# Kernel tuning notes

Measured on AMD Instinct MI355X. Metric: run time of the kernel, lower is better.

The kernel has to match this reference:

```python
import jax, jax.numpy as jnp
import numpy as np

N = 8192
IN_F = 512
OUT_F = 64
NEG_SLOPE = 0.01  # nn.LeakyReLU default
MASK_VAL = -1e9


def setup_inputs() -> dict:
    key = jax.random.key(0)
    k_h, k_adj, k_W, k_a = jax.random.split(key, 4)
    h = jax.random.normal(k_h, (N, IN_F), dtype=jnp.float32)
    adjacency = jax.random.randint(k_adj, (N, N), 0, 2, dtype=jnp.int32)
    # xavier_uniform bounds
    bW = float(np.sqrt(6.0 / (IN_F + OUT_F)))
    ba = float(np.sqrt(6.0 / (2 * OUT_F + 1)))
    W = jax.random.uniform(k_W, (IN_F, OUT_F), minval=-bW, maxval=bW, dtype=jnp.float32)
    a = jax.random.uniform(k_a, (2 * OUT_F, 1), minval=-ba, maxval=ba, dtype=jnp.float32)
    return {"h": h, "adjacency": adjacency, "W": W, "a": a}


def reference(h, adjacency, W, a):
    WH = h @ W                                  # [N, out_f]
    wh1 = WH @ a[:OUT_F, :]                     # [N, 1]
    wh2 = WH @ a[OUT_F:, :]                     # [N, 1]
    e = jax.nn.leaky_relu(wh1 + wh2.T, negative_slope=NEG_SLOPE)  # [N, N]
    attnt = jnp.where(adjacency > 0, e, jnp.float32(MASK_VAL))
    attnt = jax.nn.softmax(attnt, axis=1)       # row-wise softmax
    hfirst = attnt @ WH                         # [N, out_f]
    return jax.nn.elu(hfirst)
```

## Files before the change

kernel.cpp:

```cpp
#include <hip/hip_runtime.h>
#include <hip/hip_bf16.h>

#define N 8192
#define IN_F 512
#define OUT_F 64
#define S_SPLIT 16
#define JT (N / S_SPLIT)
#define MP 20

typedef __attribute__((ext_vector_type(8))) short short8;
typedef __attribute__((ext_vector_type(4))) float floatx4;
typedef __attribute__((ext_vector_type(4))) int intx4;

__device__ inline short f2bf(float x) {
    __hip_bfloat16 b = __float2bfloat16(x);
    return __builtin_bit_cast(short, b);
}

__global__ void k_wt(const float* __restrict__ W, short* __restrict__ WT) {
    int idx = blockIdx.x * 256 + threadIdx.x;
    int k = idx >> 6, f = idx & 63;
    WT[f * IN_F + k] = f2bf(W[k * OUT_F + f]);
}

__global__ __launch_bounds__(64) void k_wh(const float* __restrict__ h,
                                           const short* __restrict__ WT,
                                           const float* __restrict__ a,
                                           short* __restrict__ WHbT,
                                           float* __restrict__ wh1,
                                           float* __restrict__ wh2) {
    __shared__ float tile[OUT_F][17];
    int lane = threadIdx.x;
    int n = lane & 15, q = lane >> 4;
    int i0 = blockIdx.x * 16;
    int rowA = i0 + n;
    const float* hp = h + (size_t)rowA * IN_F + q * 8;
    floatx4 acc[4] = {};
    for (int k0 = 0; k0 < IN_F; k0 += 32) {
        floatx4 h0 = *(const floatx4*)(hp + k0);
        floatx4 h1 = *(const floatx4*)(hp + k0 + 4);
        short8 af;
#pragma unroll
        for (int j = 0; j < 4; j++) { af[j] = f2bf(h0[j]); af[j + 4] = f2bf(h1[j]); }
#pragma unroll
        for (int b = 0; b < 4; b++) {
            short8 bf_ = *(const short8*)(WT + (b * 16 + n) * IN_F + k0 + q * 8);
            acc[b] = __builtin_amdgcn_mfma_f32_16x16x32_bf16(af, bf_, acc[b], 0, 0, 0);
        }
    }
#pragma unroll
    for (int b = 0; b < 4; b++)
#pragma unroll
        for (int r = 0; r < 4; r++)
            tile[b * 16 + n][q * 4 + r] = acc[b][r];
    float a1v[4], a2v[4];
#pragma unroll
    for (int b = 0; b < 4; b++) { a1v[b] = a[b * 16 + n]; a2v[b] = a[OUT_F + b * 16 + n]; }
#pragma unroll
    for (int r = 0; r < 4; r++) {
        float s1 = 0.f, s2 = 0.f;
#pragma unroll
        for (int b = 0; b < 4; b++) { s1 += acc[b][r] * a1v[b]; s2 += acc[b][r] * a2v[b]; }
#pragma unroll
        for (int m = 1; m <= 8; m <<= 1) {
            s1 += __shfl_xor(s1, m, 64);
            s2 += __shfl_xor(s2, m, 64);
        }
        if (n == 0) {
            wh1[i0 + q * 4 + r] = s1;
            wh2[i0 + q * 4 + r] = s2;
        }
    }
    __syncthreads();
    const float* tc = tile[lane];
    short8 s0, s1v;
#pragma unroll
    for (int k = 0; k < 8; k++) { s0[k] = f2bf(tc[k]); s1v[k] = f2bf(tc[k + 8]); }
    *(short8*)(WHbT + (size_t)lane * N + i0) = s0;
    *(short8*)(WHbT + (size_t)lane * N + i0 + 8) = s1v;
}

__global__ __launch_bounds__(256) void k_attn(const int* __restrict__ adj,
                                              const short* __restrict__ WHbT,
                                              const float* __restrict__ wh1,
                                              const float* __restrict__ wh2,
                                              float* __restrict__ num_part,
                                              float* __restrict__ den_part) {
    __shared__ unsigned ldsm[4 * 64 * MP];
    int tid = threadIdx.x;
    int w = tid >> 6;
    int lane = tid & 63;
    int n = lane & 15, q = lane >> 4;
    int split = blockIdx.y;
    int j0 = split * JT;
    int i0 = blockIdx.x * 256 + w * 64;

    unsigned* mym = ldsm + w * 64 * MP;
    for (int rr = 0; rr < 64; rr += 2) {
#pragma unroll
        for (int u = 0; u < 2; u++) {
            const int* p = adj + (size_t)(i0 + rr + u) * N + j0 + lane;
            unsigned long long m0 = __ballot(p[0]   > 0);
            unsigned long long m1 = __ballot(p[64]  > 0);
            unsigned long long m2 = __ballot(p[128] > 0);
            unsigned long long m3 = __ballot(p[192] > 0);
            unsigned long long m4 = __ballot(p[256] > 0);
            unsigned long long m5 = __ballot(p[320] > 0);
            unsigned long long m6 = __ballot(p[384] > 0);
            unsigned long long m7 = __ballot(p[448] > 0);
            if (lane < 16) {
                unsigned long long s0 = (lane & 2) ? m1 : m0;
                unsigned long long s1 = (lane & 2) ? m3 : m2;
                unsigned long long s2 = (lane & 2) ? m5 : m4;
                unsigned long long s3 = (lane & 2) ? m7 : m6;
                unsigned long long t0 = (lane & 4) ? s1 : s0;
                unsigned long long t1 = (lane & 4) ? s3 : s2;
                unsigned long long uq = (lane & 8) ? t1 : t0;
                unsigned dw = (lane & 1) ? (unsigned)(uq >> 32) : (unsigned)uq;
                mym[(rr + u) * MP + lane] = dw;
            }
        }
    }

    float wh1f[4];
#pragma unroll
    for (int rf = 0; rf < 4; rf++) wh1f[rf] = wh1[i0 + rf * 16 + n];

    floatx4 acc[4][4] = {};
    float dsum[4] = {0.f, 0.f, 0.f, 0.f};
    const float* w2p = wh2 + j0 + q * 8;
    const short* bp0 = WHbT + (size_t)n * N + j0 + q * 8;
    int qs = q * 8;

    for (int g = 0; g < 4; g++) {
        intx4 mrf[4];
#pragma unroll
        for (int rf = 0; rf < 4; rf++)
            mrf[rf] = *(const intx4*)(mym + (rf * 16 + n) * MP + g * 4);
#pragma unroll
        for (int d = 0; d < 4; d++) {
            int s = g * 4 + d;
            floatx4 w20 = *(const floatx4*)(w2p + s * 32);
            floatx4 w21 = *(const floatx4*)(w2p + s * 32 + 4);
            short8 bfr[4];
#pragma unroll
            for (int b = 0; b < 4; b++)
                bfr[b] = *(const short8*)(bp0 + (size_t)b * 16 * N + s * 32);
#pragma unroll
            for (int rf = 0; rf < 4; rf++) {
                unsigned md = (unsigned)mrf[rf][d];
                float p[8];
#pragma unroll
                for (int jj = 0; jj < 8; jj++) {
                    float e = wh1f[rf] + ((jj < 4) ? w20[jj] : w21[jj - 4]);
                    float el = fmaxf(e, 0.01f * e);
                    float pv = __expf(el);
                    pv = ((md >> (qs + jj)) & 1u) ? pv : 0.f;
                    p[jj] = pv;
                    dsum[rf] += pv;
                }
                short8 af;
#pragma unroll
                for (int jj = 0; jj < 8; jj++) af[jj] = f2bf(p[jj]);
#pragma unroll
                for (int b = 0; b < 4; b++)
                    acc[rf][b] = __builtin_amdgcn_mfma_f32_16x16x32_bf16(af, bfr[b], acc[rf][b], 0, 0, 0);
            }
        }
    }

#pragma unroll
    for (int rf = 0; rf < 4; rf++) {
        float d = dsum[rf];
        d += __shfl_xor(d, 16, 64);
        d += __shfl_xor(d, 32, 64);
        if (q == 0) den_part[(size_t)split * N + i0 + rf * 16 + n] = d;
    }

    float* np_ = num_part + (size_t)split * N * OUT_F;
#pragma unroll
    for (int rf = 0; rf < 4; rf++)
#pragma unroll
        for (int b = 0; b < 4; b++)
#pragma unroll
            for (int r = 0; r < 4; r++)
                np_[(size_t)(i0 + rf * 16 + q * 4 + r) * OUT_F + b * 16 + n] = acc[rf][b][r];
}

__global__ void k_final(const float* __restrict__ num_part,
                        const float* __restrict__ den_part,
                        float* __restrict__ out) {
    int idx = blockIdx.x * 256 + threadIdx.x;
    int row = idx >> 6;
    float s = 0.f, d = 0.f;
#pragma unroll
    for (int sp = 0; sp < S_SPLIT; sp++) {
        s += num_part[(size_t)sp * N * OUT_F + idx];
        d += den_part[sp * N + row];
    }
    float x = s / d;
    out[idx] = (x > 0.f) ? x : (__expf(x) - 1.f);
}

extern "C" void kernel_launch(void* const* d_in, const int* in_sizes, int n_in,
                              void* d_out, int out_size, void* d_ws, size_t ws_size,
                              hipStream_t stream) {
    const float* h = (const float*)d_in[0];
    const int* adj = (const int*)d_in[1];
    const float* W = (const float*)d_in[2];
    const float* a = (const float*)d_in[3];
    float* out = (float*)d_out;

    char* ws = (char*)d_ws;
    short* WHbT  = (short*)(ws);
    short* WT    = (short*)(ws + (size_t)(1 << 20));
    float* wh1   = (float*)(ws + (size_t)(1 << 20) + (64 << 10));
    float* wh2   = wh1 + N;
    float* num_p = (float*)(ws + (size_t)(16 << 20));
    float* den_p = (float*)(ws + (size_t)(48 << 20));

    k_wt<<<dim3(128), dim3(256), 0, stream>>>(W, WT);
    k_wh<<<dim3(N / 16), dim3(64), 0, stream>>>(h, WT, a, WHbT, wh1, wh2);
    k_attn<<<dim3(N / 256, S_SPLIT), dim3(256), 0, stream>>>(adj, WHbT, wh1, wh2,
                                                             num_p, den_p);
    k_final<<<dim3((N * OUT_F) / 256), dim3(256), 0, stream>>>(num_p, den_p, out);
}
```

Measured before the change: 433.1 us.

## Shrink attention tiles to 16 rows per wave, compute denominator via MFMA, use exp2

Each wave of the attention kernel now covers 16 rows instead of 64, so the grid is four times larger, giving more blocks in flight and less register pressure. The row-sum denominator is computed with an extra MFMA against a vector of bf16 ones, replacing the scalar accumulations and shuffles. The scores are prescaled by log2(e) so the kernel can call the native exp2. The trade-off is that each WHbT and wh2 fragment is reused across fewer rows, so those loads are repeated more often. The denominator now sums the bf16-rounded probabilities, which keeps it consistent with the numerator.

After: 443.4 us. 1.02x slower.

```diff
diff --git a/kernel.cpp b/kernel.cpp
--- a/kernel.cpp
+++ b/kernel.cpp
@@ -6,11 +6,12 @@
 #define OUT_F 64
 #define S_SPLIT 16
 #define JT (N / S_SPLIT)
-#define MP 20
+#define LOG2E 1.4426950408889634f
 
 typedef __attribute__((ext_vector_type(8))) short short8;
 typedef __attribute__((ext_vector_type(4))) float floatx4;
 typedef __attribute__((ext_vector_type(4))) int intx4;
+typedef unsigned long long ull;
 
 __device__ inline short f2bf(float x) {
     __hip_bfloat16 b = __float2bfloat16(x);
@@ -27,8 +28,8 @@
                                            const short* __restrict__ WT,
                                            const float* __restrict__ a,
                                            short* __restrict__ WHbT,
-                                           float* __restrict__ wh1,
-                                           float* __restrict__ wh2) {
+                                           float* __restrict__ wh1s,
+                                           float* __restrict__ wh2s) {
     __shared__ float tile[OUT_F][17];
     int lane = threadIdx.x;
     int n = lane & 15, q = lane >> 4;
@@ -67,8 +68,8 @@
             s2 += __shfl_xor(s2, m, 64);
         }
         if (n == 0) {
-            wh1[i0 + q * 4 + r] = s1;
-            wh2[i0 + q * 4 + r] = s2;
+            wh1s[i0 + q * 4 + r] = s1 * LOG2E;
+            wh2s[i0 + q * 4 + r] = s2 * LOG2E;
         }
     }
     __syncthreads();
@@ -82,109 +83,87 @@
 
 __global__ __launch_bounds__(256) void k_attn(const int* __restrict__ adj,
                                               const short* __restrict__ WHbT,
-                                              const float* __restrict__ wh1,
-                                              const float* __restrict__ wh2,
+                                              const float* __restrict__ wh1s,
+                                              const float* __restrict__ wh2s,
                                               float* __restrict__ num_part,
                                               float* __restrict__ den_part) {
-    __shared__ unsigned ldsm[4 * 64 * MP];
+    __shared__ unsigned ldsm[4 * 16 * 17];
     int tid = threadIdx.x;
     int w = tid >> 6;
     int lane = tid & 63;
     int n = lane & 15, q = lane >> 4;
     int split = blockIdx.y;
     int j0 = split * JT;
-    int i0 = blockIdx.x * 256 + w * 64;
-
-    unsigned* mym = ldsm + w * 64 * MP;
-    for (int rr = 0; rr < 64; rr += 2) {
-#pragma unroll
-        for (int u = 0; u < 2; u++) {
-            const int* p = adj + (size_t)(i0 + rr + u) * N + j0 + lane;
-            unsigned long long m0 = __ballot(p[0]   > 0);
-            unsigned long long m1 = __ballot(p[64]  > 0);
-            unsigned long long m2 = __ballot(p[128] > 0);
-            unsigned long long m3 = __ballot(p[192] > 0);
-            unsigned long long m4 = __ballot(p[256] > 0);
-            unsigned long long m5 = __ballot(p[320] > 0);
-            unsigned long long m6 = __ballot(p[384] > 0);
-            unsigned long long m7 = __ballot(p[448] > 0);
-            if (lane < 16) {
-                unsigned long long s0 = (lane & 2) ? m1 : m0;
-                unsigned long long s1 = (lane & 2) ? m3 : m2;
-                unsigned long long s2 = (lane & 2) ? m5 : m4;
-                unsigned long long s3 = (lane & 2) ? m7 : m6;
-                unsigned long long t0 = (lane & 4) ? s1 : s0;
-                unsigned long long t1 = (lane & 4) ? s3 : s2;
-                unsigned long long uq = (lane & 8) ? t1 : t0;
-                unsigned dw = (lane & 1) ? (unsigned)(uq >> 32) : (unsigned)uq;
-                mym[(rr + u) * MP + lane] = dw;
-            }
-        }
-    }
-
-    float wh1f[4];
-#pragma unroll
-    for (int rf = 0; rf < 4; rf++) wh1f[rf] = wh1[i0 + rf * 16 + n];
-
-    floatx4 acc[4][4] = {};
-    float dsum[4] = {0.f, 0.f, 0.f, 0.f};
-    const float* w2p = wh2 + j0 + q * 8;
+    int i0 = (blockIdx.x * 4 + w) * 16;
+    unsigned* mym = ldsm + w * 16 * 17;
+
+    for (int r = 0; r < 16; r++) {
+        const int* p = adj + (size_t)(i0 + r) * N + j0 + lane;
+        ull m0 = __ballot(p[0]   > 0);
+        ull m1 = __ballot(p[64]  > 0);
+        ull m2 = __ballot(p[128] > 0);
+        ull m3 = __ballot(p[192] > 0);
+        ull m4 = __ballot(p[256] > 0);
+        ull m5 = __ballot(p[320] > 0);
+        ull m6 = __ballot(p[384] > 0);
+        ull m7 = __ballot(p[448] > 0);
+        if (lane < 16) {
+            ull s0 = (lane & 2) ? m1 : m0;
+            ull s1 = (lane & 2) ? m3 : m2;
+            ull s2 = (lane & 2) ? m5 : m4;
+            ull s3 = (lane & 2) ? m7 : m6;
+            ull t0 = (lane & 4) ? s1 : s0;
+            ull t1 = (lane & 4) ? s3 : s2;
+            ull u  = (lane & 8) ? t1 : t0;
+            unsigned dw = (lane & 1) ? (unsigned)(u >> 32) : (unsigned)u;
+            mym[r * 17 + lane] = dw;
+        }
+    }
+
+    float wh1f = wh1s[i0 + n];
+    floatx4 acc[4] = {};
+    floatx4 accd = {};
     const short* bp0 = WHbT + (size_t)n * N + j0 + q * 8;
+    const float* w2p = wh2s + j0 + q * 8;
     int qs = q * 8;
-
-    for (int g = 0; g < 4; g++) {
-        intx4 mrf[4];
-#pragma unroll
-        for (int rf = 0; rf < 4; rf++)
-            mrf[rf] = *(const intx4*)(mym + (rf * 16 + n) * MP + g * 4);
-#pragma unroll
-        for (int d = 0; d < 4; d++) {
-            int s = g * 4 + d;
-            floatx4 w20 = *(const floatx4*)(w2p + s * 32);
-            floatx4 w21 = *(const floatx4*)(w2p + s * 32 + 4);
-            short8 bfr[4];
-#pragma unroll
-            for (int b = 0; b < 4; b++)
-                bfr[b] = *(const short8*)(bp0 + (size_t)b * 16 * N + s * 32);
-#pragma unroll
-            for (int rf = 0; rf < 4; rf++) {
-                unsigned md = (unsigned)mrf[rf][d];
-                float p[8];
-#pragma unroll
-                for (int jj = 0; jj < 8; jj++) {
-                    float e = wh1f[rf] + ((jj < 4) ? w20[jj] : w21[jj - 4]);
-                    float el = fmaxf(e, 0.01f * e);
-                    float pv = __expf(el);
-                    pv = ((md >> (qs + jj)) & 1u) ? pv : 0.f;
-                    p[jj] = pv;
-                    dsum[rf] += pv;
-                }
-                short8 af;
-#pragma unroll
-                for (int jj = 0; jj < 8; jj++) af[jj] = f2bf(p[jj]);
-#pragma unroll
-                for (int b = 0; b < 4; b++)
-                    acc[rf][b] = __builtin_amdgcn_mfma_f32_16x16x32_bf16(af, bfr[b], acc[rf][b], 0, 0, 0);
-            }
-        }
-    }
-
-#pragma unroll
-    for (int rf = 0; rf < 4; rf++) {
-        float d = dsum[rf];
-        d += __shfl_xor(d, 16, 64);
-        d += __shfl_xor(d, 32, 64);
-        if (q == 0) den_part[(size_t)split * N + i0 + rf * 16 + n] = d;
-    }
-
+    short8 ones;
+#pragma unroll
+    for (int k = 0; k < 8; k++) ones[k] = (short)0x3F80;
+
+    for (int s = 0; s < 16; s++) {
+        short8 bfr[4];
+#pragma unroll
+        for (int b = 0; b < 4; b++)
+            bfr[b] = *(const short8*)(bp0 + (size_t)b * 16 * N + s * 32);
+        unsigned md = mym[n * 17 + s];
+        floatx4 w20 = *(const floatx4*)(w2p + s * 32);
+        floatx4 w21 = *(const floatx4*)(w2p + s * 32 + 4);
+
+        short8 af;
+#pragma unroll
+        for (int jj = 0; jj < 8; jj++) {
+            float x = wh1f + ((jj < 4) ? w20[jj] : w21[jj - 4]);
+            float t = fmaxf(x, 0.01f * x);
+            float e = __builtin_amdgcn_exp2f(t);
+            af[jj] = f2bf(((md >> (qs + jj)) & 1u) ? e : 0.f);
+        }
+#pragma unroll
+        for (int b = 0; b < 4; b++)
+            acc[b] = __builtin_amdgcn_mfma_f32_16x16x32_bf16(af, bfr[b], acc[b], 0, 0, 0);
+        accd = __builtin_amdgcn_mfma_f32_16x16x32_bf16(af, ones, accd, 0, 0, 0);
+    }
+
+    if (n == 0) {
+#pragma unroll
+        for (int r = 0; r < 4; r++)
+            den_part[(size_t)split * N + i0 + q * 4 + r] = accd[r];
+    }
     float* np_ = num_part + (size_t)split * N * OUT_F;
 #pragma unroll
-    for (int rf = 0; rf < 4; rf++)
-#pragma unroll
-        for (int b = 0; b < 4; b++)
-#pragma unroll
-            for (int r = 0; r < 4; r++)
-                np_[(size_t)(i0 + rf * 16 + q * 4 + r) * OUT_F + b * 16 + n] = acc[rf][b][r];
+    for (int b = 0; b < 4; b++)
+#pragma unroll
+        for (int r = 0; r < 4; r++)
+            np_[(size_t)(i0 + q * 4 + r) * OUT_F + b * 16 + n] = acc[b][r];
 }
 
 __global__ void k_final(const float* __restrict__ num_part,
@@ -214,14 +193,14 @@
     char* ws = (char*)d_ws;
     short* WHbT  = (short*)(ws);
     short* WT    = (short*)(ws + (size_t)(1 << 20));
-    float* wh1   = (float*)(ws + (size_t)(1 << 20) + (64 << 10));
-    float* wh2   = wh1 + N;
+    float* wh1s  = (float*)(ws + (size_t)(1 << 20) + (64 << 10));
+    float* wh2s  = wh1s + N;
     float* num_p = (float*)(ws + (size_t)(16 << 20));
     float* den_p = (float*)(ws + (size_t)(48 << 20));
 
     k_wt<<<dim3(128), dim3(256), 0, stream>>>(W, WT);
-    k_wh<<<dim3(N / 16), dim3(64), 0, stream>>>(h, WT, a, WHbT, wh1, wh2);
-    k_attn<<<dim3(N / 256, S_SPLIT), dim3(256), 0, stream>>>(adj, WHbT, wh1, wh2,
-                                                             num_p, den_p);
+    k_wh<<<dim3(N / 16), dim3(64), 0, stream>>>(h, WT, a, WHbT, wh1s, wh2s);
+    k_attn<<<dim3(N / 64, S_SPLIT), dim3(256), 0, stream>>>(adj, WHbT, wh1s, wh2s,
+                                                            num_p, den_p);
     k_final<<<dim3((N * OUT_F) / 256), dim3(256), 0, stream>>>(num_p, den_p, out);
 }
```
